# Optimization experiments

Measured on AMD Instinct MI355X. Metric: run time of the kernel, lower is better.

Reference implementation:

```python
import jax, jax.numpy as jnp
import numpy as np

ROI = (8, 8)          # local window (kh, kw)
H = 768
W = 768
C = ROI[0] * ROI[1]   # 64 channels == prod(roi), required by the local conv
N_LAYERS = 4          # n_decoder_layers
LN_EPS = 1e-6         # flax.linen.LayerNorm default


def setup_inputs() -> dict:
    key = jax.random.key(0)
    k0, k1, k2 = jax.random.split(key, 3)
    x = jax.random.normal(k0, (H, W, C), jnp.float32)  # post-FPN feature map
    Ws = jax.random.normal(k1, (N_LAYERS, C, C), jnp.float32) / np.float32(np.sqrt(C))
    bs = jnp.zeros((N_LAYERS, C), jnp.float32)
    ln_scale = jnp.ones((N_LAYERS, C), jnp.float32)
    ln_bias = jnp.zeros((N_LAYERS, C), jnp.float32)
    w_out = jax.random.normal(k2, (C, 1), jnp.float32) / np.float32(np.sqrt(C))
    b_out = jnp.zeros((1,), jnp.float32)
    return {"x": x, "Ws": Ws, "bs": bs, "ln_scale": ln_scale,
            "ln_bias": ln_bias, "w_out": w_out, "b_out": b_out}


def att(x, weights):
    # out[i,j,c] = sum_{di,dj} xpad[i+di, j+dj, c] * weights[i, j, di*kw+dj]
    # Equivalent to the original per-channel lax.scan over
    # conv_general_dilated_local (window ordering row-major, 'same' padding),
    # but batched over all C channels at once via shifted-slice accumulation
    # instead of materializing the (H, W, 64, C) patch tensor.
    kh, kw = ROI
    pt, pb = (kh - 1) // 2, kh - 1 - (kh - 1) // 2  # 'SAME' pad for even kernel: (3, 4)
    pl, pr = (kw - 1) // 2, kw - 1 - (kw - 1) // 2
    xpad = jnp.pad(x, ((pt, pb), (pl, pr), (0, 0)))

    def body(acc, k):
        di = k // kw
        dj = k % kw
        patch = jax.lax.dynamic_slice(xpad, (di, dj, 0), (H, W, C))
        return acc + patch * weights[:, :, k][:, :, None], None

    acc, _ = jax.lax.scan(body, jnp.zeros_like(x), jnp.arange(kh * kw))
    return acc


def layer_norm(x, scale, bias):
    mu = jnp.mean(x, axis=-1, keepdims=True)
    var = jnp.mean(jnp.square(x - mu), axis=-1, keepdims=True)
    return (x - mu) * jax.lax.rsqrt(var + LN_EPS) * scale + bias


def reference(x, Ws, bs, ln_scale, ln_bias, w_out, b_out):
    weights = jax.nn.sigmoid(x)            # spatially-varying local-conv weights
    x0 = att(x, weights)                   # (H, W, C)
    for i in range(N_LAYERS):              # MLP decoder stack
        x0 = jax.nn.relu(x0 @ Ws[i] + bs[i])
        x0 = layer_norm(x0, ln_scale[i], ln_bias[i])
    out = x0 @ w_out + b_out               # (H, W, 1)
    return (x0, out)
```

## Files before the change

### kernel.cpp

```cpp
#include <hip/hip_runtime.h>
#include <hip/hip_bf16.h>


#define HH 768
#define WW 768
#define HWPX (HH*WW)

typedef __attribute__((ext_vector_type(8))) short short8;
typedef __attribute__((ext_vector_type(8))) _Float16 half8;
typedef __attribute__((ext_vector_type(4))) float f32x4;
typedef __attribute__((ext_vector_type(16))) float f32x16;

union hcvt { _Float16 h; ushort u; };
__device__ __forceinline__ ushort f2h(float f) { hcvt c; c.h = (_Float16)f; return c.u; }
__device__ __forceinline__ float sigmoidf(float v) { return 1.f / (1.f + __expf(-v)); }

__device__ __forceinline__ int goff(int row, int g) {
  return (row << 8) + ((g ^ (row & 31)) << 3);
}
__device__ __forceinline__ int eoff(int row, int k) {
  return (row << 8) + (((k >> 3) ^ (row & 31)) << 3) + (k & 7);
}

__global__ __launch_bounds__(256)
void prep_wf(const float* __restrict__ Ws, const float* __restrict__ bs,
             const float* __restrict__ lns, const float* __restrict__ lnb,
             ushort* __restrict__ Wfg) {
  const int L = threadIdx.x >> 6, co = threadIdx.x & 63;
  float bias = bs[L * 64 + co];
  float colsum = 0.f;
  ushort* row = Wfg + (size_t)(L * 64 + co) * 80;
  for (int ci = 0; ci < 64; ++ci) {
    const float w = Ws[((L * 64 + ci) << 6) + co];
    const float sc = (L > 0) ? lns[(L - 1) * 64 + ci] : 1.f;
    const float wp = sc * w;
    if (L > 0) bias += lnb[(L - 1) * 64 + ci] * w;
    colsum += wp;
    row[ci] = f2h(wp);
  }
  row[64] = f2h(bias);
  row[65] = f2h(colsum);
  for (int q = 66; q < 80; ++q) row[q] = 0;
}

template<bool F16OUT>
__global__ __launch_bounds__(512, 4)
void att_k1(const float* __restrict__ x, void* __restrict__ attout) {
  __shared__ __align__(16) ushort Mb[64 * 256];
  __shared__ __align__(16) ushort Xb[64 * 256];
  __shared__ __align__(16) float  scr[4 * 4 * 64 * 4];
  const int tid = threadIdx.x;
  const int lane = tid & 63, w = tid >> 6;
  const int l15 = lane & 15;
  const int l31 = lane & 31, lh = lane >> 5;
  const int ot = w & 3;
  const int pb = ot >> 1, cb2 = ot & 1;
  const int kh = w >> 2;

  {
    const short8 z8 = {0,0,0,0,0,0,0,0};
    #pragma unroll
    for (int i = 0; i < 4; ++i)
      *reinterpret_cast<short8*>(&Mb[(tid + i * 512) * 8]) = z8;
  }

  const int b = blockIdx.x;
  const int tbase = (b & 7) * 1152 + (b >> 3) * 18;
  const int p  = (w & 3) * 16 + l15;
  const int pr = p >> 3, pc = p & 7;
  const int cb = ((kh << 2) + (lane >> 4 & 3)) << 3;
  const int kr0 = pr + (cb >> 3);

  float4 cv[2];
  float Rv[2][8];
  float Lv[2][8];
  short8 rs[2];

  auto issue_loads = [&](int ti, int tj, bool fresh, bool fast) {
    {
      const float* cp = x + ((size_t)((ti + pr) * WW + (tj + pc)) << 6) + cb;
      cv[0] = *reinterpret_cast<const float4*>(cp);
      cv[1] = *reinterpret_cast<const float4*>(cp + 4);
    }
    #pragma unroll
    for (int i = 0; i < 2; ++i) {
      const int r = w + 8 * i;
      if (r < 15) {
        if (fast) {
          const int gr = ti + r - 3;
          const float* rowp = x + ((size_t)(gr * WW + tj) << 6) + lane;
          #pragma unroll
          for (int s = 0; s < 8; ++s)
            Rv[i][s] = rowp[(5 + s) << 6];
          if (fresh) {
            #pragma unroll
            for (int s = 0; s < 8; ++s)
              Lv[i][s] = rowp[(s - 3) << 6];
          }
        } else {
          const int gr = min(max(ti + r - 3, 0), HH - 1);
          const float* rowp = x + ((size_t)gr * WW << 6) + lane;
          #pragma unroll
          for (int s = 0; s < 8; ++s) {
            const int gc = min(max(tj + 5 + s, 0), WW - 1);
            Rv[i][s] = rowp[(size_t)gc << 6];
          }
          if (fresh) {
            #pragma unroll
            for (int s = 0; s < 8; ++s) {
              const int gc = min(max(tj - 3 + s, 0), WW - 1);
              Lv[i][s] = rowp[(size_t)gc << 6];
            }
          }
        }
      }
    }
  };

  auto write_lds = [&](int ti, int tj, bool fresh, bool fast) {
    #pragma unroll
    for (int qd = 0; qd < 2; ++qd) {
      const float vs[4] = {cv[qd].x, cv[qd].y, cv[qd].z, cv[qd].w};
      #pragma unroll
      for (int j = 0; j < 4; ++j) {
        const int k = (kr0 << 4) + pc + qd * 4 + j;
        Mb[eoff(p, k)] = f2h(sigmoidf(vs[j]));
      }
    }
    #pragma unroll
    for (int i = 0; i < 2; ++i) {
      const int r = w + 8 * i;
      if (r < 15) {
        short8 left8, right8;
        if (fast) {
          if (fresh) {
            #pragma unroll
            for (int s = 0; s < 8; ++s) left8[s] = (short)f2h(Lv[i][s]);
          } else {
            left8 = rs[i];
          }
          #pragma unroll
          for (int s = 0; s < 8; ++s) right8[s] = (short)f2h(Rv[i][s]);
        } else {
          const int gr = ti + r - 3;
          const bool rok = (unsigned)gr < (unsigned)HH;
          if (fresh) {
            #pragma unroll
            for (int s = 0; s < 8; ++s) {
              const int j = tj - 3 + s;
              const bool ok = rok && ((unsigned)j < (unsigned)WW);
              left8[s] = (short)f2h(ok ? Lv[i][s] : 0.f);
            }
          } else {
            left8 = rs[i];
          }
          #pragma unroll
          for (int s = 0; s < 8; ++s) {
            const int j = tj + 5 + s;
            const bool ok = rok && ((unsigned)j < (unsigned)WW);
            right8[s] = (short)f2h(ok ? Rv[i][s] : 0.f);
          }
        }
        *reinterpret_cast<short8*>(&Xb[goff(lane, 2 * r)])     = left8;
        *reinterpret_cast<short8*>(&Xb[goff(lane, 2 * r + 1)]) = right8;
        rs[i] = right8;
      }
    }
  };

  f32x16 acc;
  int pti = 0, ptj = 0;

  auto store_acc = [&](int ti, int tj) {
    const int ch = cb2 * 32 + l31;
    #pragma unroll
    for (int q = 0; q < 4; ++q) {
      const size_t gpx0 = (size_t)(ti + 4 * pb + q) * WW + (tj + 4 * lh);
      if (F16OUT) {
        ushort* bp = (ushort*)attout + (gpx0 << 6) + ch;
        #pragma unroll
        for (int j = 0; j < 4; ++j) bp[j << 6] = f2h(acc[q * 4 + j]);
      } else {
        float* bp = (float*)attout + (gpx0 << 6) + ch;
        #pragma unroll
        for (int j = 0; j < 4; ++j) bp[j << 6] = acc[q * 4 + j];
      }
    }
  };

  auto tile_fast = [](int ti, int tj, bool fresh) {
    return (ti != 0) && (ti != HH - 8) && (tj != WW - 8) && (!fresh || tj != 0);
  };

  {
    const int ti0 = (tbase / 96) * 8, tj0 = (tbase % 96) * 8;
    issue_loads(ti0, tj0, true, tile_fast(ti0, tj0, true));
  }

  for (int t18 = 0; t18 < 18; ++t18) {
    const int tile = tbase + t18;
    const int ti = (tile / 96) * 8, tj = (tile % 96) * 8;
    const bool fresh = (t18 == 0) || (tj == 0);

    __syncthreads();
    if (kh == 0 && t18 > 0) {
      #pragma unroll
      for (int q = 0; q < 4; ++q) {
        const float4 pv = *reinterpret_cast<const float4*>(&scr[ot * 1024 + q * 256 + lane * 4]);
        acc[q * 4 + 0] += pv.x; acc[q * 4 + 1] += pv.y;
        acc[q * 4 + 2] += pv.z; acc[q * 4 + 3] += pv.w;
      }
    }
    write_lds(ti, tj, fresh, tile_fast(ti, tj, fresh));
    __syncthreads();
    if (kh == 0 && t18 > 0) store_acc(pti, ptj);
    if (t18 < 17) {
      const int nt = tile + 1;
      const int nti = (nt / 96) * 8, ntj = (nt % 96) * 8;
      const bool nfresh = (nt % 96) == 0;
      issue_loads(nti, ntj, nfresh, tile_fast(nti, ntj, nfresh));
    }

    acc = (f32x16){0,0,0,0,0,0,0,0,0,0,0,0,0,0,0,0};
    const int ks0 = kh ? 7 : 0, ks1 = kh ? 15 : 7;
    #pragma unroll 8
    for (int ks = ks0; ks < ks1; ++ks) {
      const int g = 2 * ks + lh;
      const half8 a  = *reinterpret_cast<const half8*>(&Mb[goff(pb * 32 + l31, g)]);
      const half8 bb = *reinterpret_cast<const half8*>(&Xb[goff(cb2 * 32 + l31, g)]);
      acc = __builtin_amdgcn_mfma_f32_32x32x16_f16(a, bb, acc, 0, 0, 0);
    }
    if (kh == 1) {
      #pragma unroll
      for (int q = 0; q < 4; ++q) {
        float4 pv;
        pv.x = acc[q * 4 + 0]; pv.y = acc[q * 4 + 1];
        pv.z = acc[q * 4 + 2]; pv.w = acc[q * 4 + 3];
        *reinterpret_cast<float4*>(&scr[ot * 1024 + q * 256 + lane * 4]) = pv;
      }
    }
    pti = ti; ptj = tj;
  }
  __syncthreads();
  if (kh == 0) {
    #pragma unroll
    for (int q = 0; q < 4; ++q) {
      const float4 pv = *reinterpret_cast<const float4*>(&scr[ot * 1024 + q * 256 + lane * 4]);
      acc[q * 4 + 0] += pv.x; acc[q * 4 + 1] += pv.y;
      acc[q * 4 + 2] += pv.z; acc[q * 4 + 3] += pv.w;
    }
    store_acc(pti, ptj);
  }
}

__device__ __forceinline__ float zsel(const f32x16& z0, const f32x16& z1, int nb, int idx) {
  return nb ? z1[idx] : z0[idx];
}

template<bool F16IN>
__global__ __launch_bounds__(512, 2)
void mlp_k2(const void* attv, const ushort* __restrict__ Wfg,
            const float* __restrict__ lns, const float* __restrict__ lnb,
            const float* __restrict__ w_out, const float* __restrict__ b_out,
            float* x0_out, float* __restrict__ out1) {
  __shared__ __align__(16) ushort act[8][32 * 88];
  __shared__ __align__(16) ushort kpat[16];
  const int tid = threadIdx.x;
  const int lane = tid & 63, wid = tid >> 6;
  const int l31 = lane & 31, lh = lane >> 5;

  for (int idx = tid; idx < 256; idx += 512) {
    ushort* rp = &act[idx >> 5][(idx & 31) * 88];
    for (int q = 64; q < 88; ++q) rp[q] = 0;
    rp[64] = 0x3C00;
  }
  if (tid < 16) kpat[tid] = (tid == 0) ? (ushort)0x3C00 : (ushort)0;

  float sc3[2][4][4], lb3[2][4][4], wo3[2][4][4];
  #pragma unroll
  for (int nb = 0; nb < 2; ++nb)
    #pragma unroll
    for (int hi = 0; hi < 4; ++hi)
      #pragma unroll
      for (int j = 0; j < 4; ++j) {
        const int ch = nb * 32 + hi * 8 + lh * 4 + j;
        sc3[nb][hi][j] = lns[192 + ch];
        lb3[nb][hi][j] = lnb[192 + ch];
        wo3[nb][hi][j] = w_out[ch];
      }
  const float b0s = b_out[0];
  const ushort* wr0 = Wfg + (size_t)l31 * 80 + lh * 8;
  __syncthreads();

  ushort* const myact = act[wid];

  for (int it = 0; it < 5; ++it) {
    const int chunk = it * 512 + (int)blockIdx.x;
    if (chunk >= 2304) break;
    const int px = (chunk * 8 + wid) * 32 + l31;

    half8 bfr[5];
    if (F16IN) {
      const ushort* ap = (const ushort*)attv + ((size_t)px << 6) + lh * 8;
      #pragma unroll
      for (int g = 0; g < 4; ++g)
        bfr[g] = *reinterpret_cast<const half8*>(ap + g * 16);
    } else {
      const float* ap = (const float*)attv + ((size_t)px << 6) + lh * 8;
      #pragma unroll
      for (int g = 0; g < 4; ++g) {
        const float4 fa = *reinterpret_cast<const float4*>(ap + g * 16);
        const float4 fb = *reinterpret_cast<const float4*>(ap + g * 16 + 4);
        half8 h;
        h[0]=(_Float16)fa.x; h[1]=(_Float16)fa.y; h[2]=(_Float16)fa.z; h[3]=(_Float16)fa.w;
        h[4]=(_Float16)fb.x; h[5]=(_Float16)fb.y; h[6]=(_Float16)fb.z; h[7]=(_Float16)fb.w;
        bfr[g] = h;
      }
    }
    bfr[4] = *reinterpret_cast<const half8*>(&kpat[lh * 8]);

    f32x16 z0, z1;
    float mu = 0.f, rstd = 1.f;
    #pragma unroll
    for (int L = 0; L < 4; ++L) {
      if (L > 0) {
        #pragma unroll
        for (int g = 0; g < 5; ++g)
          bfr[g] = *reinterpret_cast<const half8*>(&myact[l31 * 88 + g * 16 + lh * 8]);
      }
      z0 = (f32x16){0,0,0,0,0,0,0,0,0,0,0,0,0,0,0,0};
      z1 = (f32x16){0,0,0,0,0,0,0,0,0,0,0,0,0,0,0,0};
      const ushort* wL = wr0 + (size_t)(L * 64) * 80;
      #pragma unroll
      for (int g = 0; g < 5; ++g) {
        const half8 a0 = *reinterpret_cast<const half8*>(wL + g * 16);
        const half8 a1 = *reinterpret_cast<const half8*>(wL + (size_t)32 * 80 + g * 16);
        z0 = __builtin_amdgcn_mfma_f32_32x32x16_f16(a0, bfr[g], z0, 0, 0, 0);
        z1 = __builtin_amdgcn_mfma_f32_32x32x16_f16(a1, bfr[g], z1, 0, 0, 0);
      }
      float sp[4] = {0.f, 0.f, 0.f, 0.f}, qp[4] = {0.f, 0.f, 0.f, 0.f};
      #pragma unroll
      for (int r = 0; r < 16; ++r) {
        const float v0 = fmaxf(z0[r], 0.f); z0[r] = v0;
        const float v1 = fmaxf(z1[r], 0.f); z1[r] = v1;
        sp[r & 3] += v0 + v1;
        qp[r & 3] += v0 * v0 + v1 * v1;
      }
      float s = (sp[0] + sp[1]) + (sp[2] + sp[3]);
      float qq = (qp[0] + qp[1]) + (qp[2] + qp[3]);
      s  += __shfl_xor(s, 32, 64);
      qq += __shfl_xor(qq, 32, 64);
      mu = s * 0.015625f;
      const float var = qq * 0.015625f - mu * mu;
      rstd = rsqrtf(var + 1e-6f);
      if (L < 3) {
        #pragma unroll
        for (int nb = 0; nb < 2; ++nb)
          #pragma unroll
          for (int hi = 0; hi < 4; ++hi) {
            ushort4 pk;
            pk.x = f2h(rstd * zsel(z0, z1, nb, hi * 4 + 0));
            pk.y = f2h(rstd * zsel(z0, z1, nb, hi * 4 + 1));
            pk.z = f2h(rstd * zsel(z0, z1, nb, hi * 4 + 2));
            pk.w = f2h(rstd * zsel(z0, z1, nb, hi * 4 + 3));
            *reinterpret_cast<ushort4*>(&myact[l31 * 88 + nb * 32 + hi * 8 + lh * 4]) = pk;
          }
        if (lh == 0) myact[l31 * 88 + 65] = f2h(-(mu * rstd));
      }
    }

    const float t = mu * rstd;
    float part0 = 0.f, part1 = 0.f;
    #pragma unroll
    for (int nb = 0; nb < 2; ++nb)
      #pragma unroll
      for (int hi = 0; hi < 4; ++hi) {
        f32x4 yv;
        #pragma unroll
        for (int j = 0; j < 4; ++j) {
          const float v = zsel(z0, z1, nb, hi * 4 + j);
          const float y = v * (rstd * sc3[nb][hi][j]) + (lb3[nb][hi][j] - t * sc3[nb][hi][j]);
          yv[j] = y;
          if (j & 1) part1 += y * wo3[nb][hi][j];
          else       part0 += y * wo3[nb][hi][j];
        }
        *reinterpret_cast<f32x4*>(&x0_out[((size_t)px << 6) + nb * 32 + hi * 8 + lh * 4]) = yv;
      }
    float part = part0 + part1;
    part += __shfl_xor(part, 32, 64);
    if (lh == 0) out1[px] = part + b0s;
  }
}

extern "C" void kernel_launch(void* const* d_in, const int* in_sizes, int n_in,
                              void* d_out, int out_size, void* d_ws, size_t ws_size,
                              hipStream_t stream) {
  const float* x     = (const float*)d_in[0];
  const float* Ws    = (const float*)d_in[1];
  const float* bs    = (const float*)d_in[2];
  const float* lns   = (const float*)d_in[3];
  const float* lnbv  = (const float*)d_in[4];
  const float* w_out = (const float*)d_in[5];
  const float* b_out = (const float*)d_in[6];
  float* x0_out = (float*)d_out;
  float* out1   = x0_out + (size_t)HWPX * 64;

  const size_t attBytes = (size_t)HWPX * 64 * sizeof(ushort);
  if (ws_size >= attBytes + 65536) {
    ushort* atth = (ushort*)d_ws;
    ushort* Wfg  = (ushort*)((char*)d_ws + attBytes);
    prep_wf<<<1, 256, 0, stream>>>(Ws, bs, lns, lnbv, Wfg);
    att_k1<true><<<512, 512, 0, stream>>>(x, atth);
    mlp_k2<true><<<512, 512, 0, stream>>>(atth, Wfg, lns, lnbv,
                                          w_out, b_out, x0_out, out1);
  } else {
    ushort* Wfg = (ushort*)d_ws;
    prep_wf<<<1, 256, 0, stream>>>(Ws, bs, lns, lnbv, Wfg);
    att_k1<false><<<512, 512, 0, stream>>>(x, d_out);
    mlp_k2<false><<<512, 512, 0, stream>>>(d_out, Wfg, lns, lnbv,
                                           w_out, b_out, x0_out, out1);
  }
}
```

Before: 203.8 us.

## Stage MLP weights in LDS and pass activations between layers via lane shuffles

Loads all four layers' fused fp16 weight matrices into shared memory once per block, instead of reading them from global memory for every pixel chunk. The per-wave activation staging buffer is removed. Inter-layer activations are now repacked into the MFMA B-operand registers with cross-half-wave shuffles, replacing an LDS write/read round trip. This trades LDS traffic and barriers for extra shuffle and select instructions. It also raises LDS use per block, which may affect occupancy.

New measurement: 301.2 us. 47.8% more time.

```diff
diff --git a/kernel.cpp b/kernel.cpp
--- a/kernel.cpp
+++ b/kernel.cpp
@@ -14,6 +14,10 @@
 union hcvt { _Float16 h; ushort u; };
 __device__ __forceinline__ ushort f2h(float f) { hcvt c; c.h = (_Float16)f; return c.u; }
 __device__ __forceinline__ float sigmoidf(float v) { return 1.f / (1.f + __expf(-v)); }
+__device__ __forceinline__ uint pack_h2(float a, float b) {
+  return (uint)f2h(a) | ((uint)f2h(b) << 16);
+}
+union h8u4 { half8 h; uint u[4]; };
 
 __device__ __forceinline__ int goff(int row, int g) {
   return (row << 8) + ((g ^ (row & 31)) << 3);
@@ -263,18 +267,16 @@
             const float* __restrict__ lns, const float* __restrict__ lnb,
             const float* __restrict__ w_out, const float* __restrict__ b_out,
             float* x0_out, float* __restrict__ out1) {
-  __shared__ __align__(16) ushort act[8][32 * 88];
-  __shared__ __align__(16) ushort kpat[16];
+  __shared__ __align__(16) ushort wt[4 * 64 * 88];
   const int tid = threadIdx.x;
   const int lane = tid & 63, wid = tid >> 6;
   const int l31 = lane & 31, lh = lane >> 5;
 
-  for (int idx = tid; idx < 256; idx += 512) {
-    ushort* rp = &act[idx >> 5][(idx & 31) * 88];
-    for (int q = 64; q < 88; ++q) rp[q] = 0;
-    rp[64] = 0x3C00;
-  }
-  if (tid < 16) kpat[tid] = (tid == 0) ? (ushort)0x3C00 : (ushort)0;
+  for (int idx = tid; idx < 4 * 64 * 10; idx += 512) {
+    const int row = idx / 10, q = idx - row * 10;
+    *reinterpret_cast<uint4*>(&wt[row * 88 + q * 8]) =
+        *reinterpret_cast<const uint4*>(&Wfg[(size_t)row * 80 + q * 8]);
+  }
 
   float sc3[2][4][4], lb3[2][4][4], wo3[2][4][4];
   #pragma unroll
@@ -289,10 +291,7 @@
         wo3[nb][hi][j] = w_out[ch];
       }
   const float b0s = b_out[0];
-  const ushort* wr0 = Wfg + (size_t)l31 * 80 + lh * 8;
   __syncthreads();
-
-  ushort* const myact = act[wid];
 
   for (int it = 0; it < 5; ++it) {
     const int chunk = it * 512 + (int)blockIdx.x;
@@ -317,24 +316,23 @@
         bfr[g] = h;
       }
     }
-    bfr[4] = *reinterpret_cast<const half8*>(&kpat[lh * 8]);
+    {
+      h8u4 u4;
+      u4.u[0] = lh ? 0u : 0x3C00u;
+      u4.u[1] = 0u; u4.u[2] = 0u; u4.u[3] = 0u;
+      bfr[4] = u4.h;
+    }
 
     f32x16 z0, z1;
     float mu = 0.f, rstd = 1.f;
     #pragma unroll
     for (int L = 0; L < 4; ++L) {
-      if (L > 0) {
-        #pragma unroll
-        for (int g = 0; g < 5; ++g)
-          bfr[g] = *reinterpret_cast<const half8*>(&myact[l31 * 88 + g * 16 + lh * 8]);
-      }
       z0 = (f32x16){0,0,0,0,0,0,0,0,0,0,0,0,0,0,0,0};
       z1 = (f32x16){0,0,0,0,0,0,0,0,0,0,0,0,0,0,0,0};
-      const ushort* wL = wr0 + (size_t)(L * 64) * 80;
       #pragma unroll
       for (int g = 0; g < 5; ++g) {
-        const half8 a0 = *reinterpret_cast<const half8*>(wL + g * 16);
-        const half8 a1 = *reinterpret_cast<const half8*>(wL + (size_t)32 * 80 + g * 16);
+        const half8 a0 = *reinterpret_cast<const half8*>(&wt[(L * 64      + l31) * 88 + g * 16 + lh * 8]);
+        const half8 a1 = *reinterpret_cast<const half8*>(&wt[(L * 64 + 32 + l31) * 88 + g * 16 + lh * 8]);
         z0 = __builtin_amdgcn_mfma_f32_32x32x16_f16(a0, bfr[g], z0, 0, 0, 0);
         z1 = __builtin_amdgcn_mfma_f32_32x32x16_f16(a1, bfr[g], z1, 0, 0, 0);
       }
@@ -353,19 +351,35 @@
       mu = s * 0.015625f;
       const float var = qq * 0.015625f - mu * mu;
       rstd = rsqrtf(var + 1e-6f);
+
       if (L < 3) {
         #pragma unroll
         for (int nb = 0; nb < 2; ++nb)
           #pragma unroll
-          for (int hi = 0; hi < 4; ++hi) {
-            ushort4 pk;
-            pk.x = f2h(rstd * zsel(z0, z1, nb, hi * 4 + 0));
-            pk.y = f2h(rstd * zsel(z0, z1, nb, hi * 4 + 1));
-            pk.z = f2h(rstd * zsel(z0, z1, nb, hi * 4 + 2));
-            pk.w = f2h(rstd * zsel(z0, z1, nb, hi * 4 + 3));
-            *reinterpret_cast<ushort4*>(&myact[l31 * 88 + nb * 32 + hi * 8 + lh * 4]) = pk;
-          }
-        if (lh == 0) myact[l31 * 88 + 65] = f2h(-(mu * rstd));
+          for (int q = 0; q < 2; ++q) {
+            const int hi_own  = 2 * q + lh;
+            const int hi_send = 2 * q + (lh ^ 1);
+            const uint own0 = pack_h2(rstd * zsel(z0, z1, nb, hi_own * 4 + 0),
+                                      rstd * zsel(z0, z1, nb, hi_own * 4 + 1));
+            const uint own1 = pack_h2(rstd * zsel(z0, z1, nb, hi_own * 4 + 2),
+                                      rstd * zsel(z0, z1, nb, hi_own * 4 + 3));
+            const uint snd0 = pack_h2(rstd * zsel(z0, z1, nb, hi_send * 4 + 0),
+                                      rstd * zsel(z0, z1, nb, hi_send * 4 + 1));
+            const uint snd1 = pack_h2(rstd * zsel(z0, z1, nb, hi_send * 4 + 2),
+                                      rstd * zsel(z0, z1, nb, hi_send * 4 + 3));
+            const uint rcv0 = __shfl_xor(snd0, 32, 64);
+            const uint rcv1 = __shfl_xor(snd1, 32, 64);
+            h8u4 u;
+            u.u[0] = lh ? rcv0 : own0;
+            u.u[1] = lh ? rcv1 : own1;
+            u.u[2] = lh ? own0 : rcv0;
+            u.u[3] = lh ? own1 : rcv1;
+            bfr[2 * nb + q] = u.h;
+          }
+        h8u4 u4;
+        u4.u[0] = lh ? 0u : (0x3C00u | ((uint)f2h(-(mu * rstd)) << 16));
+        u4.u[1] = 0u; u4.u[2] = 0u; u4.u[3] = 0u;
+        bfr[4] = u4.h;
       }
     }
 
```
